# Performance work log

Hardware: AMD Instinct MI355X
Metric: run time of the kernel (lower is better)

Reference implementation:

```python
import jax, jax.numpy as jnp
import numpy as np

N_NODES = 50000
N_EDGES = 1600000
D_FEAT = 128
EPS = 1e-12  # matches F.normalize clamp_min eps


def setup_inputs() -> dict:
    key = jax.random.key(0)
    k1, k2 = jax.random.split(key)
    x = jax.random.normal(k1, (N_NODES, D_FEAT), dtype=jnp.float32)
    beta = jnp.ones((1,), dtype=jnp.float32)  # AGNNConv learnable scalar, init 1.0
    edge_index = jax.random.randint(k2, (2, N_EDGES), 0, N_NODES, dtype=jnp.int64)
    return {"x": x, "beta": beta, "edge_index": edge_index}


def reference(x, beta, edge_index):
    N = x.shape[0]
    # AGNNConv default add_self_loops=True
    loop = jnp.arange(N, dtype=edge_index.dtype)
    src = jnp.concatenate([edge_index[0], loop])  # j (source / message sender)
    dst = jnp.concatenate([edge_index[1], loop])  # i (target / aggregator)

    # cosine-similarity attention logits per edge, scaled by beta
    xn = x * jax.lax.rsqrt(jnp.maximum(jnp.sum(x * x, axis=-1, keepdims=True), EPS * EPS))
    logits = beta[0] * jnp.sum(xn[src] * xn[dst], axis=-1)  # [E+N]

    # segment softmax over incoming edges of each target node
    m = jax.ops.segment_max(logits, dst, num_segments=N)
    m = jax.lax.stop_gradient(m)
    e = jnp.exp(logits - m[dst])
    s = jax.ops.segment_sum(e, dst, num_segments=N)
    alpha = e / s[dst]  # self-loops guarantee s > 0

    # scatter-aggregate messages alpha_e * x_src
    out = jax.ops.segment_sum(alpha[:, None] * x[src], dst, num_segments=N)

    # wrapper: activation (relu); normalization=False; dropout p=0 -> identity
    return jax.nn.relu(out)
```

## Files before the change

### kernel.cpp

```cpp
#include <hip/hip_runtime.h>

#define NN 50000
#define NE 1600000
#define DF 128
#define NB 250
#define BSZ 200
#define NWG 256
#define CHK 6250
#define NBN 12500

static __device__ __forceinline__ float bflo(unsigned int u) {
    unsigned int v = u << 16; float f; __builtin_memcpy(&f, &v, 4); return f;
}
static __device__ __forceinline__ float bfhi(unsigned int u) {
    unsigned int v = u & 0xFFFF0000u; float f; __builtin_memcpy(&f, &v, 4); return f;
}
static __device__ __forceinline__ unsigned int f2bf(float f) {
    unsigned int u; __builtin_memcpy(&u, &f, 4);
    u += 0x7FFFu + ((u >> 16) & 1u);
    return u >> 16;
}

static __device__ __forceinline__ int block_excl_scan(int v, int t, int* wsum4) {
    int lane = t & 63, wv = t >> 6;
    int s = v;
    #pragma unroll
    for (int off = 1; off < 64; off <<= 1) {
        int u = __shfl_up(s, off);
        if (lane >= off) s += u;
    }
    if (lane == 63) wsum4[wv] = s;
    __syncthreads();
    int add = 0;
    #pragma unroll
    for (int w = 0; w < 4; ++w) add += (w < wv) ? wsum4[w] : 0;
    __syncthreads();
    return s + add - v;
}

__global__ void k_norm_count(const float* __restrict__ x,
                             const int* __restrict__ ei,
                             unsigned int* __restrict__ xn_bf,
                             float* __restrict__ norm,
                             int* __restrict__ whist) {
    if (blockIdx.x < NBN) {
        int wave = (blockIdx.x * 256 + threadIdx.x) >> 6;
        int lane = threadIdx.x & 63;
        float2 v = ((const float2*)(x + (size_t)wave * DF))[lane];
        float ss = v.x * v.x + v.y * v.y;
        #pragma unroll
        for (int m = 1; m < 64; m <<= 1) ss += __shfl_xor(ss, m);
        float rinv = rsqrtf(fmaxf(ss, 1e-24f));
        xn_bf[(size_t)wave * 64 + lane] = (f2bf(v.y * rinv) << 16) | f2bf(v.x * rinv);
        if (lane == 0) norm[wave] = ss * rinv;
    } else {
        __shared__ int h[NB];
        int wg = blockIdx.x - NBN, t = threadIdx.x;
        if (t < NB) h[t] = 0;
        __syncthreads();
        const int* dstp = ei + NE + wg * CHK;
        for (int i = t; i < CHK; i += 256) atomicAdd(&h[dstp[i] / BSZ], 1);
        __syncthreads();
        if (t < NB) whist[wg * NB + t] = h[t];
    }
}

__global__ void k_scan(int* __restrict__ whist, int* __restrict__ btotal) {
    __shared__ int wsum4[4];
    int b = blockIdx.x, t = threadIdx.x;
    int v = whist[t * NB + b];
    int excl = block_excl_scan(v, t, wsum4);
    whist[t * NB + b] = excl;
    if (t == NWG - 1) btotal[b] = excl + v;
}

__global__ void k_part(const int* __restrict__ ei, const int* __restrict__ whist,
                       const int* __restrict__ btotal, unsigned int* __restrict__ pairs) {
    __shared__ int wsum4[4];
    __shared__ int cur[NB];
    int wg = blockIdx.x, t = threadIdx.x;
    int v = (t < NB) ? btotal[t] : 0;
    int base = block_excl_scan(v, t, wsum4);
    if (t < NB) cur[t] = base + whist[wg * NB + t];
    __syncthreads();
    int c0 = wg * CHK;
    for (int i = t; i < CHK; i += 256) {
        int src = ei[c0 + i];
        int dst = ei[NE + c0 + i];
        int b = dst / BSZ;
        int pos = atomicAdd(&cur[b], 1);
        pairs[pos] = ((unsigned int)(dst - b * BSZ) << 16) | (unsigned int)src;
    }
}

__global__ void k_build(const unsigned int* __restrict__ pairs,
                        const int* __restrict__ btotal,
                        const float* __restrict__ norm,
                        int* __restrict__ row_ptr, unsigned int* __restrict__ col) {
    __shared__ int wsum4[4];
    __shared__ int h[BSZ];
    __shared__ int sbase, send;
    int b = blockIdx.x, t = threadIdx.x;
    int v = (t < NB) ? btotal[t] : 0;
    int base_t = block_excl_scan(v, t, wsum4);
    if (t == b) { sbase = base_t; send = base_t + v; }
    if (t < BSZ) h[t] = 0;
    __syncthreads();
    int base = sbase, end = send;
    for (int i = base + t; i < end; i += 256) atomicAdd(&h[pairs[i] >> 16], 1);
    __syncthreads();
    int own = (t < BSZ) ? h[t] : 0;
    __syncthreads();
    int excl = block_excl_scan(own, t, wsum4);
    if (t < BSZ) {
        row_ptr[b * BSZ + t] = base + excl;
        h[t] = base + excl;
    }
    if (b == 0 && t == 0) row_ptr[NN] = NE;
    __syncthreads();
    for (int i = base + t; i < end; i += 256) {
        unsigned int p = pairs[i];
        unsigned int src = p & 0xFFFFu;
        int pos = atomicAdd(&h[p >> 16], 1);
        col[pos] = (f2bf(norm[src]) << 16) | src;
    }
}

__global__ void k_gather(const unsigned int* __restrict__ xn_bf,
                         const float* __restrict__ norm,
                         const int* __restrict__ row_ptr,
                         const unsigned int* __restrict__ col,
                         const float* __restrict__ beta_p,
                         float* __restrict__ out) {
    int wave = (blockIdx.x * blockDim.x + threadIdx.x) >> 6;
    int lane = threadIdx.x & 63;
    if (wave >= NN) return;
    int j = lane & 15;
    int g = lane >> 4;
    float beta = beta_p[0];
    float c = -fabsf(beta);

    uint4 du = ((const uint4*)(xn_bf + (size_t)wave * 64))[j];
    float xd[8];
    #pragma unroll
    for (int q = 0; q < 4; ++q) {
        unsigned int u = (&du.x)[q];
        xd[2 * q]     = bflo(u);
        xd[2 * q + 1] = bfhi(u);
    }

    float acc[8] = {0.f, 0.f, 0.f, 0.f, 0.f, 0.f, 0.f, 0.f};
    float ssum = 0.f;
    int b0 = row_ptr[wave], b1 = row_ptr[wave + 1];

    int k = b0 + g;
    int kA = (k     < b1) ? k     : 0;
    int kB = (k + 4 < b1) ? k + 4 : 0;
    unsigned int pA = col[kA];
    unsigned int pB = col[kB];
    uint4 rA = ((const uint4*)(xn_bf + (size_t)(pA & 0xFFFFu) * 64))[j];
    uint4 rB = ((const uint4*)(xn_bf + (size_t)(pB & 0xFFFFu) * 64))[j];

    for (; k < b1; k += 8) {
        int kC = (k +  8 < b1) ? k +  8 : 0;
        int kD = (k + 12 < b1) ? k + 12 : 0;
        unsigned int pC = col[kC];
        unsigned int pD = col[kD];
        uint4 rC = ((const uint4*)(xn_bf + (size_t)(pC & 0xFFFFu) * 64))[j];
        uint4 rD = ((const uint4*)(xn_bf + (size_t)(pD & 0xFFFFu) * 64))[j];

        {
            float xs[8];
            #pragma unroll
            for (int q = 0; q < 4; ++q) {
                unsigned int u = (&rA.x)[q];
                xs[2 * q]     = bflo(u);
                xs[2 * q + 1] = bfhi(u);
            }
            float dot = 0.f;
            #pragma unroll
            for (int q = 0; q < 8; ++q) dot = fmaf(xd[q], xs[q], dot);
            dot += __shfl_xor(dot, 1);
            dot += __shfl_xor(dot, 2);
            dot += __shfl_xor(dot, 4);
            dot += __shfl_xor(dot, 8);
            float e = __expf(fmaf(beta, dot, c));
            ssum += e;
            float w = e * bfhi(pA);
            #pragma unroll
            for (int q = 0; q < 8; ++q) acc[q] = fmaf(w, xs[q], acc[q]);
        }
        {
            float xs[8];
            #pragma unroll
            for (int q = 0; q < 4; ++q) {
                unsigned int u = (&rB.x)[q];
                xs[2 * q]     = bflo(u);
                xs[2 * q + 1] = bfhi(u);
            }
            float dot = 0.f;
            #pragma unroll
            for (int q = 0; q < 8; ++q) dot = fmaf(xd[q], xs[q], dot);
            dot += __shfl_xor(dot, 1);
            dot += __shfl_xor(dot, 2);
            dot += __shfl_xor(dot, 4);
            dot += __shfl_xor(dot, 8);
            float e = __expf(fmaf(beta, dot, c));
            e = (k + 4 < b1) ? e : 0.f;
            ssum += e;
            float w = e * bfhi(pB);
            #pragma unroll
            for (int q = 0; q < 8; ++q) acc[q] = fmaf(w, xs[q], acc[q]);
        }
        pA = pC; pB = pD; rA = rC; rB = rD;
    }

    ssum += __shfl_xor(ssum, 16);
    ssum += __shfl_xor(ssum, 32);
    #pragma unroll
    for (int q = 0; q < 8; ++q) {
        acc[q] += __shfl_xor(acc[q], 16);
        acc[q] += __shfl_xor(acc[q], 32);
    }

    float e_self = __expf(beta + c);
    ssum += e_self;
    float wsl = e_self * norm[wave];
    #pragma unroll
    for (int q = 0; q < 8; ++q) acc[q] = fmaf(wsl, xd[q], acc[q]);

    if (g == 0) {
        float inv = 1.0f / ssum;
        float4 o0, o1;
        o0.x = fmaxf(0.f, acc[0] * inv); o0.y = fmaxf(0.f, acc[1] * inv);
        o0.z = fmaxf(0.f, acc[2] * inv); o0.w = fmaxf(0.f, acc[3] * inv);
        o1.x = fmaxf(0.f, acc[4] * inv); o1.y = fmaxf(0.f, acc[5] * inv);
        o1.z = fmaxf(0.f, acc[6] * inv); o1.w = fmaxf(0.f, acc[7] * inv);
        float4* op = (float4*)(out + (size_t)wave * DF + 8 * j);
        op[0] = o0;
        op[1] = o1;
    }
}

extern "C" void kernel_launch(void* const* d_in, const int* in_sizes, int n_in,
                              void* d_out, int out_size, void* d_ws, size_t ws_size,
                              hipStream_t stream) {
    const float* x    = (const float*)d_in[0];
    const float* beta = (const float*)d_in[1];
    const int*   ei   = (const int*)d_in[2];
    float*       out  = (float*)d_out;

    char* ws = (char*)d_ws;
    unsigned int* xn_bf = (unsigned int*)ws;
    float* norm    = (float*)(ws + 12800000);
    int*   whist   = (int*)  (ws + 13000000);
    int*   btotal  = (int*)  (ws + 13256000);
    int*   row_ptr = (int*)  (ws + 13257024);
    unsigned int* pairs = (unsigned int*)(ws + 13457040);
    unsigned int* col   = (unsigned int*)(ws + 19857040);

    k_norm_count<<<NBN + NWG, 256, 0, stream>>>(x, ei, xn_bf, norm, whist);
    k_scan      <<<NB,        NWG, 0, stream>>>(whist, btotal);
    k_part      <<<NWG,       256, 0, stream>>>(ei, whist, btotal, pairs);
    k_build     <<<NB,        256, 0, stream>>>(pairs, btotal, norm, row_ptr, col);
    k_gather    <<<(NN * 64 + 255) / 256, 256, 0, stream>>>(xn_bf, norm, row_ptr, col, beta, out);
}
```

Measured before the change: 177.5 us.

## Fuse all stages into one cooperative persistent kernel with grid syncs

After: 669.2 us. +276.9%, slower.

```diff
diff --git a/kernel.cpp b/kernel.cpp
--- a/kernel.cpp
+++ b/kernel.cpp
@@ -1,4 +1,7 @@
 #include <hip/hip_runtime.h>
+#include <hip/hip_cooperative_groups.h>
+
+namespace cg = cooperative_groups;
 
 #define NN 50000
 #define NE 1600000
@@ -7,7 +10,6 @@
 #define BSZ 200
 #define NWG 256
 #define CHK 6250
-#define NBN 12500
 
 static __device__ __forceinline__ float bflo(unsigned int u) {
     unsigned int v = u << 16; float f; __builtin_memcpy(&f, &v, 4); return f;
@@ -38,207 +40,210 @@
     return s + add - v;
 }
 
-__global__ void k_norm_count(const float* __restrict__ x,
-                             const int* __restrict__ ei,
-                             unsigned int* __restrict__ xn_bf,
-                             float* __restrict__ norm,
-                             int* __restrict__ whist) {
-    if (blockIdx.x < NBN) {
-        int wave = (blockIdx.x * 256 + threadIdx.x) >> 6;
-        int lane = threadIdx.x & 63;
-        float2 v = ((const float2*)(x + (size_t)wave * DF))[lane];
-        float ss = v.x * v.x + v.y * v.y;
-        #pragma unroll
-        for (int m = 1; m < 64; m <<= 1) ss += __shfl_xor(ss, m);
-        float rinv = rsqrtf(fmaxf(ss, 1e-24f));
-        xn_bf[(size_t)wave * 64 + lane] = (f2bf(v.y * rinv) << 16) | f2bf(v.x * rinv);
-        if (lane == 0) norm[wave] = ss * rinv;
-    } else {
-        __shared__ int h[NB];
-        int wg = blockIdx.x - NBN, t = threadIdx.x;
-        if (t < NB) h[t] = 0;
-        __syncthreads();
-        const int* dstp = ei + NE + wg * CHK;
-        for (int i = t; i < CHK; i += 256) atomicAdd(&h[dstp[i] / BSZ], 1);
-        __syncthreads();
-        if (t < NB) whist[wg * NB + t] = h[t];
-    }
-}
-
-__global__ void k_scan(int* __restrict__ whist, int* __restrict__ btotal) {
+__global__ __launch_bounds__(256, 8)
+void k_mega(const float* __restrict__ x, const float* __restrict__ beta_p,
+            const int* __restrict__ ei,
+            unsigned int* __restrict__ xn_bf, float* __restrict__ norm,
+            int* __restrict__ whist, int* __restrict__ btotal,
+            int* __restrict__ row_ptr, unsigned int* __restrict__ pairs,
+            unsigned int* __restrict__ col, float* __restrict__ out) {
+    cg::grid_group grid = cg::this_grid();
     __shared__ int wsum4[4];
-    int b = blockIdx.x, t = threadIdx.x;
-    int v = whist[t * NB + b];
-    int excl = block_excl_scan(v, t, wsum4);
-    whist[t * NB + b] = excl;
-    if (t == NWG - 1) btotal[b] = excl + v;
-}
-
-__global__ void k_part(const int* __restrict__ ei, const int* __restrict__ whist,
-                       const int* __restrict__ btotal, unsigned int* __restrict__ pairs) {
-    __shared__ int wsum4[4];
-    __shared__ int cur[NB];
-    int wg = blockIdx.x, t = threadIdx.x;
-    int v = (t < NB) ? btotal[t] : 0;
-    int base = block_excl_scan(v, t, wsum4);
-    if (t < NB) cur[t] = base + whist[wg * NB + t];
-    __syncthreads();
-    int c0 = wg * CHK;
-    for (int i = t; i < CHK; i += 256) {
-        int src = ei[c0 + i];
-        int dst = ei[NE + c0 + i];
-        int b = dst / BSZ;
-        int pos = atomicAdd(&cur[b], 1);
-        pairs[pos] = ((unsigned int)(dst - b * BSZ) << 16) | (unsigned int)src;
-    }
-}
-
-__global__ void k_build(const unsigned int* __restrict__ pairs,
-                        const int* __restrict__ btotal,
-                        const float* __restrict__ norm,
-                        int* __restrict__ row_ptr, unsigned int* __restrict__ col) {
-    __shared__ int wsum4[4];
-    __shared__ int h[BSZ];
+    __shared__ int smem[NB];
     __shared__ int sbase, send;
-    int b = blockIdx.x, t = threadIdx.x;
-    int v = (t < NB) ? btotal[t] : 0;
-    int base_t = block_excl_scan(v, t, wsum4);
-    if (t == b) { sbase = base_t; send = base_t + v; }
-    if (t < BSZ) h[t] = 0;
-    __syncthreads();
-    int base = sbase, end = send;
-    for (int i = base + t; i < end; i += 256) atomicAdd(&h[pairs[i] >> 16], 1);
-    __syncthreads();
-    int own = (t < BSZ) ? h[t] : 0;
-    __syncthreads();
-    int excl = block_excl_scan(own, t, wsum4);
-    if (t < BSZ) {
-        row_ptr[b * BSZ + t] = base + excl;
-        h[t] = base + excl;
-    }
-    if (b == 0 && t == 0) row_ptr[NN] = NE;
-    __syncthreads();
-    for (int i = base + t; i < end; i += 256) {
-        unsigned int p = pairs[i];
-        unsigned int src = p & 0xFFFFu;
-        int pos = atomicAdd(&h[p >> 16], 1);
-        col[pos] = (f2bf(norm[src]) << 16) | src;
-    }
-}
-
-__global__ void k_gather(const unsigned int* __restrict__ xn_bf,
-                         const float* __restrict__ norm,
-                         const int* __restrict__ row_ptr,
-                         const unsigned int* __restrict__ col,
-                         const float* __restrict__ beta_p,
-                         float* __restrict__ out) {
-    int wave = (blockIdx.x * blockDim.x + threadIdx.x) >> 6;
-    int lane = threadIdx.x & 63;
-    if (wave >= NN) return;
-    int j = lane & 15;
-    int g = lane >> 4;
-    float beta = beta_p[0];
-    float c = -fabsf(beta);
-
-    uint4 du = ((const uint4*)(xn_bf + (size_t)wave * 64))[j];
-    float xd[8];
-    #pragma unroll
-    for (int q = 0; q < 4; ++q) {
-        unsigned int u = (&du.x)[q];
-        xd[2 * q]     = bflo(u);
-        xd[2 * q + 1] = bfhi(u);
-    }
-
-    float acc[8] = {0.f, 0.f, 0.f, 0.f, 0.f, 0.f, 0.f, 0.f};
-    float ssum = 0.f;
-    int b0 = row_ptr[wave], b1 = row_ptr[wave + 1];
-
-    int k = b0 + g;
-    int kA = (k     < b1) ? k     : 0;
-    int kB = (k + 4 < b1) ? k + 4 : 0;
-    unsigned int pA = col[kA];
-    unsigned int pB = col[kB];
-    uint4 rA = ((const uint4*)(xn_bf + (size_t)(pA & 0xFFFFu) * 64))[j];
-    uint4 rB = ((const uint4*)(xn_bf + (size_t)(pB & 0xFFFFu) * 64))[j];
-
-    for (; k < b1; k += 8) {
-        int kC = (k +  8 < b1) ? k +  8 : 0;
-        int kD = (k + 12 < b1) ? k + 12 : 0;
-        unsigned int pC = col[kC];
-        unsigned int pD = col[kD];
-        uint4 rC = ((const uint4*)(xn_bf + (size_t)(pC & 0xFFFFu) * 64))[j];
-        uint4 rD = ((const uint4*)(xn_bf + (size_t)(pD & 0xFFFFu) * 64))[j];
-
-        {
-            float xs[8];
+    const int t = threadIdx.x;
+    const int bid = blockIdx.x;
+    const int nblk = gridDim.x;
+
+    {
+        bool split = (nblk >= NWG + 256);
+        bool do_count = (bid < NWG);
+        bool do_norm = split ? (bid >= NWG) : true;
+        if (do_norm) {
+            int nbid = split ? bid - NWG : bid;
+            int nnb  = split ? nblk - NWG : nblk;
+            int lane = t & 63;
+            int w0 = nbid * 4 + (t >> 6);
+            int wstep = nnb * 4;
+            for (int node = w0; node < NN; node += wstep) {
+                float2 v = ((const float2*)(x + (size_t)node * DF))[lane];
+                float ss = v.x * v.x + v.y * v.y;
+                #pragma unroll
+                for (int m = 1; m < 64; m <<= 1) ss += __shfl_xor(ss, m);
+                float rinv = rsqrtf(fmaxf(ss, 1e-24f));
+                xn_bf[(size_t)node * 64 + lane] = (f2bf(v.y * rinv) << 16) | f2bf(v.x * rinv);
+                if (lane == 0) norm[node] = ss * rinv;
+            }
+        }
+        if (do_count) {
+            if (t < NB) smem[t] = 0;
+            __syncthreads();
+            const int* dstp = ei + NE + bid * CHK;
+            for (int i = t; i < CHK; i += 256) atomicAdd(&smem[dstp[i] / BSZ], 1);
+            __syncthreads();
+            if (t < NB) whist[bid * NB + t] = smem[t];
+        }
+    }
+    grid.sync();
+
+    if (bid < NB) {
+        int v = whist[t * NB + bid];
+        int excl = block_excl_scan(v, t, wsum4);
+        whist[t * NB + bid] = excl;
+        if (t == NWG - 1) btotal[bid] = excl + v;
+    }
+    grid.sync();
+
+    if (bid < NWG) {
+        int v = (t < NB) ? btotal[t] : 0;
+        int base = block_excl_scan(v, t, wsum4);
+        if (t < NB) smem[t] = base + whist[bid * NB + t];
+        __syncthreads();
+        int c0 = bid * CHK;
+        for (int i = t; i < CHK; i += 256) {
+            int src = ei[c0 + i];
+            int dst = ei[NE + c0 + i];
+            int b = dst / BSZ;
+            int pos = atomicAdd(&smem[b], 1);
+            pairs[pos] = ((unsigned int)(dst - b * BSZ) << 16) | (unsigned int)src;
+        }
+    }
+    grid.sync();
+
+    if (bid < NB) {
+        int v = (t < NB) ? btotal[t] : 0;
+        int base_t = block_excl_scan(v, t, wsum4);
+        if (t == bid) { sbase = base_t; send = base_t + v; }
+        if (t < BSZ) smem[t] = 0;
+        __syncthreads();
+        int base = sbase, end = send;
+        for (int i = base + t; i < end; i += 256) atomicAdd(&smem[pairs[i] >> 16], 1);
+        __syncthreads();
+        int own = (t < BSZ) ? smem[t] : 0;
+        __syncthreads();
+        int excl = block_excl_scan(own, t, wsum4);
+        if (t < BSZ) {
+            row_ptr[bid * BSZ + t] = base + excl;
+            smem[t] = base + excl;
+        }
+        if (bid == 0 && t == 0) row_ptr[NN] = NE;
+        __syncthreads();
+        for (int i = base + t; i < end; i += 256) {
+            unsigned int p = pairs[i];
+            unsigned int src = p & 0xFFFFu;
+            int pos = atomicAdd(&smem[p >> 16], 1);
+            col[pos] = (f2bf(norm[src]) << 16) | src;
+        }
+    }
+    grid.sync();
+
+    {
+        int lane = t & 63;
+        int j = lane & 15;
+        int g = lane >> 4;
+        float beta = beta_p[0];
+        float c = -fabsf(beta);
+        int gw = bid * 4 + (t >> 6);
+        int gstep = nblk * 4;
+        for (int node = gw; node < NN; node += gstep) {
+            uint4 du = ((const uint4*)(xn_bf + (size_t)node * 64))[j];
+            float xd[8];
             #pragma unroll
             for (int q = 0; q < 4; ++q) {
-                unsigned int u = (&rA.x)[q];
-                xs[2 * q]     = bflo(u);
-                xs[2 * q + 1] = bfhi(u);
-            }
-            float dot = 0.f;
+                unsigned int u = (&du.x)[q];
+                xd[2 * q]     = bflo(u);
+                xd[2 * q + 1] = bfhi(u);
+            }
+            float acc[8] = {0.f, 0.f, 0.f, 0.f, 0.f, 0.f, 0.f, 0.f};
+            float ssum = 0.f;
+            int b0 = row_ptr[node], b1 = row_ptr[node + 1];
+
+            int k = b0 + g;
+            int kA = (k     < b1) ? k     : 0;
+            int kB = (k + 4 < b1) ? k + 4 : 0;
+            unsigned int pA = col[kA];
+            unsigned int pB = col[kB];
+            uint4 rA = ((const uint4*)(xn_bf + (size_t)(pA & 0xFFFFu) * 64))[j];
+            uint4 rB = ((const uint4*)(xn_bf + (size_t)(pB & 0xFFFFu) * 64))[j];
+
+            for (; k < b1; k += 8) {
+                int kC = (k +  8 < b1) ? k +  8 : 0;
+                int kD = (k + 12 < b1) ? k + 12 : 0;
+                unsigned int pC = col[kC];
+                unsigned int pD = col[kD];
+                uint4 rC = ((const uint4*)(xn_bf + (size_t)(pC & 0xFFFFu) * 64))[j];
+                uint4 rD = ((const uint4*)(xn_bf + (size_t)(pD & 0xFFFFu) * 64))[j];
+                {
+                    float xs[8];
+                    #pragma unroll
+                    for (int q = 0; q < 4; ++q) {
+                        unsigned int u = (&rA.x)[q];
+                        xs[2 * q]     = bflo(u);
+                        xs[2 * q + 1] = bfhi(u);
+                    }
+                    float dot = 0.f;
+                    #pragma unroll
+                    for (int q = 0; q < 8; ++q) dot = fmaf(xd[q], xs[q], dot);
+                    dot += __shfl_xor(dot, 1);
+                    dot += __shfl_xor(dot, 2);
+                    dot += __shfl_xor(dot, 4);
+                    dot += __shfl_xor(dot, 8);
+                    float e = __expf(fmaf(beta, dot, c));
+                    ssum += e;
+                    float w = e * bfhi(pA);
+                    #pragma unroll
+                    for (int q = 0; q < 8; ++q) acc[q] = fmaf(w, xs[q], acc[q]);
+                }
+                {
+                    float xs[8];
+                    #pragma unroll
+                    for (int q = 0; q < 4; ++q) {
+                        unsigned int u = (&rB.x)[q];
+                        xs[2 * q]     = bflo(u);
+                        xs[2 * q + 1] = bfhi(u);
+                    }
+                    float dot = 0.f;
+                    #pragma unroll
+                    for (int q = 0; q < 8; ++q) dot = fmaf(xd[q], xs[q], dot);
+                    dot += __shfl_xor(dot, 1);
+                    dot += __shfl_xor(dot, 2);
+                    dot += __shfl_xor(dot, 4);
+                    dot += __shfl_xor(dot, 8);
+                    float e = __expf(fmaf(beta, dot, c));
+                    e = (k + 4 < b1) ? e : 0.f;
+                    ssum += e;
+                    float w = e * bfhi(pB);
+                    #pragma unroll
+                    for (int q = 0; q < 8; ++q) acc[q] = fmaf(w, xs[q], acc[q]);
+                }
+                pA = pC; pB = pD; rA = rC; rB = rD;
+            }
+
+            ssum += __shfl_xor(ssum, 16);
+            ssum += __shfl_xor(ssum, 32);
             #pragma unroll
-            for (int q = 0; q < 8; ++q) dot = fmaf(xd[q], xs[q], dot);
-            dot += __shfl_xor(dot, 1);
-            dot += __shfl_xor(dot, 2);
-            dot += __shfl_xor(dot, 4);
-            dot += __shfl_xor(dot, 8);
-            float e = __expf(fmaf(beta, dot, c));
-            ssum += e;
-            float w = e * bfhi(pA);
+            for (int q = 0; q < 8; ++q) {
+                acc[q] += __shfl_xor(acc[q], 16);
+                acc[q] += __shfl_xor(acc[q], 32);
+            }
+            float e_self = __expf(beta + c);
+            ssum += e_self;
+            float wsl = e_self * norm[node];
             #pragma unroll
-            for (int q = 0; q < 8; ++q) acc[q] = fmaf(w, xs[q], acc[q]);
-        }
-        {
-            float xs[8];
-            #pragma unroll
-            for (int q = 0; q < 4; ++q) {
-                unsigned int u = (&rB.x)[q];
-                xs[2 * q]     = bflo(u);
-                xs[2 * q + 1] = bfhi(u);
-            }
-            float dot = 0.f;
-            #pragma unroll
-            for (int q = 0; q < 8; ++q) dot = fmaf(xd[q], xs[q], dot);
-            dot += __shfl_xor(dot, 1);
-            dot += __shfl_xor(dot, 2);
-            dot += __shfl_xor(dot, 4);
-            dot += __shfl_xor(dot, 8);
-            float e = __expf(fmaf(beta, dot, c));
-            e = (k + 4 < b1) ? e : 0.f;
-            ssum += e;
-            float w = e * bfhi(pB);
-            #pragma unroll
-            for (int q = 0; q < 8; ++q) acc[q] = fmaf(w, xs[q], acc[q]);
-        }
-        pA = pC; pB = pD; rA = rC; rB = rD;
-    }
-
-    ssum += __shfl_xor(ssum, 16);
-    ssum += __shfl_xor(ssum, 32);
-    #pragma unroll
-    for (int q = 0; q < 8; ++q) {
-        acc[q] += __shfl_xor(acc[q], 16);
-        acc[q] += __shfl_xor(acc[q], 32);
-    }
-
-    float e_self = __expf(beta + c);
-    ssum += e_self;
-    float wsl = e_self * norm[wave];
-    #pragma unroll
-    for (int q = 0; q < 8; ++q) acc[q] = fmaf(wsl, xd[q], acc[q]);
-
-    if (g == 0) {
-        float inv = 1.0f / ssum;
-        float4 o0, o1;
-        o0.x = fmaxf(0.f, acc[0] * inv); o0.y = fmaxf(0.f, acc[1] * inv);
-        o0.z = fmaxf(0.f, acc[2] * inv); o0.w = fmaxf(0.f, acc[3] * inv);
-        o1.x = fmaxf(0.f, acc[4] * inv); o1.y = fmaxf(0.f, acc[5] * inv);
-        o1.z = fmaxf(0.f, acc[6] * inv); o1.w = fmaxf(0.f, acc[7] * inv);
-        float4* op = (float4*)(out + (size_t)wave * DF + 8 * j);
-        op[0] = o0;
-        op[1] = o1;
+            for (int q = 0; q < 8; ++q) acc[q] = fmaf(wsl, xd[q], acc[q]);
+
+            if (g == 0) {
+                float inv = 1.0f / ssum;
+                float4 o0, o1;
+                o0.x = fmaxf(0.f, acc[0] * inv); o0.y = fmaxf(0.f, acc[1] * inv);
+                o0.z = fmaxf(0.f, acc[2] * inv); o0.w = fmaxf(0.f, acc[3] * inv);
+                o1.x = fmaxf(0.f, acc[4] * inv); o1.y = fmaxf(0.f, acc[5] * inv);
+                o1.z = fmaxf(0.f, acc[6] * inv); o1.w = fmaxf(0.f, acc[7] * inv);
+                float4* op = (float4*)(out + (size_t)node * DF + 8 * j);
+                op[0] = o0;
+                op[1] = o1;
+            }
+        }
     }
 }
 
@@ -259,9 +264,21 @@
     unsigned int* pairs = (unsigned int*)(ws + 13457040);
     unsigned int* col   = (unsigned int*)(ws + 19857040);
 
-    k_norm_count<<<NBN + NWG, 256, 0, stream>>>(x, ei, xn_bf, norm, whist);
-    k_scan      <<<NB,        NWG, 0, stream>>>(whist, btotal);
-    k_part      <<<NWG,       256, 0, stream>>>(ei, whist, btotal, pairs);
-    k_build     <<<NB,        256, 0, stream>>>(pairs, btotal, norm, row_ptr, col);
-    k_gather    <<<(NN * 64 + 255) / 256, 256, 0, stream>>>(xn_bf, norm, row_ptr, col, beta, out);
-}
+    int dev = 0;
+    hipGetDevice(&dev);
+    int nb = 0;
+    hipOccupancyMaxActiveBlocksPerMultiprocessor(&nb, (const void*)k_mega, 256, 0);
+    if (nb < 1) nb = 1;
+    int ncu = 0;
+    hipDeviceGetAttribute(&ncu, hipDeviceAttributeMultiprocessorCount, dev);
+    if (ncu < 1) ncu = 256;
+    long grid = (long)nb * ncu;
+    if (grid > 2048) grid = 2048;
+    if (grid < NWG) grid = NWG;
+
+    void* args[] = { (void*)&x, (void*)&beta, (void*)&ei,
+                     (void*)&xn_bf, (void*)&norm, (void*)&whist, (void*)&btotal,
+                     (void*)&row_ptr, (void*)&pairs, (void*)&col, (void*)&out };
+    hipLaunchCooperativeKernel((const void*)k_mega, dim3((unsigned)grid), dim3(256),
+                               args, 0, stream);
+}
```

## Fuse CSR build into gather using fixed-capacity buckets and global atomics

Applied to the files above, without the earlier changes.

Result: slower. 193.2 us (+8.8%).

```diff
diff --git a/kernel.cpp b/kernel.cpp
--- a/kernel.cpp
+++ b/kernel.cpp
@@ -3,10 +3,11 @@
 #define NN 50000
 #define NE 1600000
 #define DF 128
-#define NB 250
-#define BSZ 200
-#define NWG 256
-#define CHK 6250
+#define NB 1250
+#define BSZ 40
+#define CAP 1664
+#define NWGP 512
+#define CHKP 3125
 #define NBN 12500
 
 static __device__ __forceinline__ float bflo(unsigned int u) {
@@ -21,224 +22,192 @@
     return u >> 16;
 }
 
-static __device__ __forceinline__ int block_excl_scan(int v, int t, int* wsum4) {
-    int lane = t & 63, wv = t >> 6;
-    int s = v;
-    #pragma unroll
-    for (int off = 1; off < 64; off <<= 1) {
-        int u = __shfl_up(s, off);
-        if (lane >= off) s += u;
-    }
-    if (lane == 63) wsum4[wv] = s;
-    __syncthreads();
-    int add = 0;
-    #pragma unroll
-    for (int w = 0; w < 4; ++w) add += (w < wv) ? wsum4[w] : 0;
-    __syncthreads();
-    return s + add - v;
-}
-
-__global__ void k_norm_count(const float* __restrict__ x,
-                             const int* __restrict__ ei,
-                             unsigned int* __restrict__ xn_bf,
-                             float* __restrict__ norm,
-                             int* __restrict__ whist) {
+__global__ void k_norm_part(const float* __restrict__ x,
+                            const int* __restrict__ ei,
+                            unsigned int* __restrict__ xn_bf,
+                            float* __restrict__ norm,
+                            int* __restrict__ gcnt,
+                            unsigned int* __restrict__ pairs) {
     if (blockIdx.x < NBN) {
-        int wave = (blockIdx.x * 256 + threadIdx.x) >> 6;
+        int node = (blockIdx.x * 256 + threadIdx.x) >> 6;
         int lane = threadIdx.x & 63;
-        float2 v = ((const float2*)(x + (size_t)wave * DF))[lane];
+        float2 v = ((const float2*)(x + (size_t)node * DF))[lane];
         float ss = v.x * v.x + v.y * v.y;
         #pragma unroll
         for (int m = 1; m < 64; m <<= 1) ss += __shfl_xor(ss, m);
         float rinv = rsqrtf(fmaxf(ss, 1e-24f));
-        xn_bf[(size_t)wave * 64 + lane] = (f2bf(v.y * rinv) << 16) | f2bf(v.x * rinv);
-        if (lane == 0) norm[wave] = ss * rinv;
+        xn_bf[(size_t)node * 64 + lane] = (f2bf(v.y * rinv) << 16) | f2bf(v.x * rinv);
+        if (lane == 0) norm[node] = ss * rinv;
     } else {
         __shared__ int h[NB];
         int wg = blockIdx.x - NBN, t = threadIdx.x;
-        if (t < NB) h[t] = 0;
+        for (int i = t; i < NB; i += 256) h[i] = 0;
         __syncthreads();
-        const int* dstp = ei + NE + wg * CHK;
-        for (int i = t; i < CHK; i += 256) atomicAdd(&h[dstp[i] / BSZ], 1);
+        const int* dstp = ei + NE + wg * CHKP;
+        const int* srcp = ei + wg * CHKP;
+        for (int i = t; i < CHKP; i += 256) atomicAdd(&h[dstp[i] / BSZ], 1);
         __syncthreads();
-        if (t < NB) whist[wg * NB + t] = h[t];
-    }
-}
-
-__global__ void k_scan(int* __restrict__ whist, int* __restrict__ btotal) {
-    __shared__ int wsum4[4];
+        for (int i = t; i < NB; i += 256) {
+            int c = h[i];
+            int base = (c > 0) ? atomicAdd(&gcnt[i], c) : 0;
+            h[i] = i * CAP + base;
+        }
+        __syncthreads();
+        for (int i = t; i < CHKP; i += 256) {
+            int src = srcp[i];
+            int dst = dstp[i];
+            int b = dst / BSZ;
+            int pos = atomicAdd(&h[b], 1);
+            if (pos < (b + 1) * CAP)
+                pairs[pos] = ((unsigned int)(dst - b * BSZ) << 16) | (unsigned int)src;
+        }
+    }
+}
+
+__global__ __launch_bounds__(256)
+void k_build_gather(const unsigned int* __restrict__ xn_bf,
+                    const float* __restrict__ norm,
+                    const int* __restrict__ gcnt,
+                    const unsigned int* __restrict__ pairs,
+                    const float* __restrict__ beta_p,
+                    float* __restrict__ out) {
+    __shared__ unsigned int colL[CAP];
+    __shared__ int hist[BSZ];
+    __shared__ int rp[BSZ + 1];
     int b = blockIdx.x, t = threadIdx.x;
-    int v = whist[t * NB + b];
-    int excl = block_excl_scan(v, t, wsum4);
-    whist[t * NB + b] = excl;
-    if (t == NWG - 1) btotal[b] = excl + v;
-}
-
-__global__ void k_part(const int* __restrict__ ei, const int* __restrict__ whist,
-                       const int* __restrict__ btotal, unsigned int* __restrict__ pairs) {
-    __shared__ int wsum4[4];
-    __shared__ int cur[NB];
-    int wg = blockIdx.x, t = threadIdx.x;
-    int v = (t < NB) ? btotal[t] : 0;
-    int base = block_excl_scan(v, t, wsum4);
-    if (t < NB) cur[t] = base + whist[wg * NB + t];
-    __syncthreads();
-    int c0 = wg * CHK;
-    for (int i = t; i < CHK; i += 256) {
-        int src = ei[c0 + i];
-        int dst = ei[NE + c0 + i];
-        int b = dst / BSZ;
-        int pos = atomicAdd(&cur[b], 1);
-        pairs[pos] = ((unsigned int)(dst - b * BSZ) << 16) | (unsigned int)src;
-    }
-}
-
-__global__ void k_build(const unsigned int* __restrict__ pairs,
-                        const int* __restrict__ btotal,
-                        const float* __restrict__ norm,
-                        int* __restrict__ row_ptr, unsigned int* __restrict__ col) {
-    __shared__ int wsum4[4];
-    __shared__ int h[BSZ];
-    __shared__ int sbase, send;
-    int b = blockIdx.x, t = threadIdx.x;
-    int v = (t < NB) ? btotal[t] : 0;
-    int base_t = block_excl_scan(v, t, wsum4);
-    if (t == b) { sbase = base_t; send = base_t + v; }
-    if (t < BSZ) h[t] = 0;
-    __syncthreads();
-    int base = sbase, end = send;
-    for (int i = base + t; i < end; i += 256) atomicAdd(&h[pairs[i] >> 16], 1);
-    __syncthreads();
-    int own = (t < BSZ) ? h[t] : 0;
-    __syncthreads();
-    int excl = block_excl_scan(own, t, wsum4);
-    if (t < BSZ) {
-        row_ptr[b * BSZ + t] = base + excl;
-        h[t] = base + excl;
-    }
-    if (b == 0 && t == 0) row_ptr[NN] = NE;
-    __syncthreads();
-    for (int i = base + t; i < end; i += 256) {
-        unsigned int p = pairs[i];
+    int cnt = gcnt[b];
+    if (cnt > CAP) cnt = CAP;
+    int base = b * CAP;
+
+    if (t < BSZ) hist[t] = 0;
+    __syncthreads();
+    for (int i = t; i < cnt; i += 256) atomicAdd(&hist[pairs[base + i] >> 16], 1);
+    __syncthreads();
+    if (t < 64) {
+        int v = (t < BSZ) ? hist[t] : 0;
+        int s = v;
+        #pragma unroll
+        for (int off = 1; off < 64; off <<= 1) {
+            int u = __shfl_up(s, off);
+            if (t >= off) s += u;
+        }
+        if (t < BSZ) { rp[t + 1] = s; hist[t] = s - v; }
+        if (t == 0) rp[0] = 0;
+    }
+    __syncthreads();
+    for (int i = t; i < cnt; i += 256) {
+        unsigned int p = pairs[base + i];
         unsigned int src = p & 0xFFFFu;
-        int pos = atomicAdd(&h[p >> 16], 1);
-        col[pos] = (f2bf(norm[src]) << 16) | src;
-    }
-}
-
-__global__ void k_gather(const unsigned int* __restrict__ xn_bf,
-                         const float* __restrict__ norm,
-                         const int* __restrict__ row_ptr,
-                         const unsigned int* __restrict__ col,
-                         const float* __restrict__ beta_p,
-                         float* __restrict__ out) {
-    int wave = (blockIdx.x * blockDim.x + threadIdx.x) >> 6;
-    int lane = threadIdx.x & 63;
-    if (wave >= NN) return;
+        int pos = atomicAdd(&hist[p >> 16], 1);
+        colL[pos] = (f2bf(norm[src]) << 16) | src;
+    }
+    __syncthreads();
+
+    int lane = t & 63;
+    int w = t >> 6;
     int j = lane & 15;
     int g = lane >> 4;
     float beta = beta_p[0];
     float c = -fabsf(beta);
-
-    uint4 du = ((const uint4*)(xn_bf + (size_t)wave * 64))[j];
-    float xd[8];
-    #pragma unroll
-    for (int q = 0; q < 4; ++q) {
-        unsigned int u = (&du.x)[q];
-        xd[2 * q]     = bflo(u);
-        xd[2 * q + 1] = bfhi(u);
-    }
-
-    float acc[8] = {0.f, 0.f, 0.f, 0.f, 0.f, 0.f, 0.f, 0.f};
-    float ssum = 0.f;
-    int b0 = row_ptr[wave], b1 = row_ptr[wave + 1];
-
-    int k = b0 + g;
-    int kA = (k     < b1) ? k     : 0;
-    int kB = (k + 4 < b1) ? k + 4 : 0;
-    unsigned int pA = col[kA];
-    unsigned int pB = col[kB];
-    uint4 rA = ((const uint4*)(xn_bf + (size_t)(pA & 0xFFFFu) * 64))[j];
-    uint4 rB = ((const uint4*)(xn_bf + (size_t)(pB & 0xFFFFu) * 64))[j];
-
-    for (; k < b1; k += 8) {
-        int kC = (k +  8 < b1) ? k +  8 : 0;
-        int kD = (k + 12 < b1) ? k + 12 : 0;
-        unsigned int pC = col[kC];
-        unsigned int pD = col[kD];
-        uint4 rC = ((const uint4*)(xn_bf + (size_t)(pC & 0xFFFFu) * 64))[j];
-        uint4 rD = ((const uint4*)(xn_bf + (size_t)(pD & 0xFFFFu) * 64))[j];
-
-        {
-            float xs[8];
-            #pragma unroll
-            for (int q = 0; q < 4; ++q) {
-                unsigned int u = (&rA.x)[q];
-                xs[2 * q]     = bflo(u);
-                xs[2 * q + 1] = bfhi(u);
+    for (int ln = w; ln < BSZ; ln += 4) {
+        int node = b * BSZ + ln;
+        uint4 du = ((const uint4*)(xn_bf + (size_t)node * 64))[j];
+        float xd[8];
+        #pragma unroll
+        for (int q = 0; q < 4; ++q) {
+            unsigned int u = (&du.x)[q];
+            xd[2 * q]     = bflo(u);
+            xd[2 * q + 1] = bfhi(u);
+        }
+        float acc[8] = {0.f, 0.f, 0.f, 0.f, 0.f, 0.f, 0.f, 0.f};
+        float ssum = 0.f;
+        int b0 = rp[ln], b1 = rp[ln + 1];
+
+        int k = b0 + g;
+        int kA = (k     < b1) ? k     : 0;
+        int kB = (k + 4 < b1) ? k + 4 : 0;
+        unsigned int pA = colL[kA];
+        unsigned int pB = colL[kB];
+        uint4 rA = ((const uint4*)(xn_bf + (size_t)(pA & 0xFFFFu) * 64))[j];
+        uint4 rB = ((const uint4*)(xn_bf + (size_t)(pB & 0xFFFFu) * 64))[j];
+
+        for (; k < b1; k += 8) {
+            int kC = (k +  8 < b1) ? k +  8 : 0;
+            int kD = (k + 12 < b1) ? k + 12 : 0;
+            unsigned int pC = colL[kC];
+            unsigned int pD = colL[kD];
+            uint4 rC = ((const uint4*)(xn_bf + (size_t)(pC & 0xFFFFu) * 64))[j];
+            uint4 rD = ((const uint4*)(xn_bf + (size_t)(pD & 0xFFFFu) * 64))[j];
+            {
+                float xs[8];
+                #pragma unroll
+                for (int q = 0; q < 4; ++q) {
+                    unsigned int u = (&rA.x)[q];
+                    xs[2 * q]     = bflo(u);
+                    xs[2 * q + 1] = bfhi(u);
+                }
+                float dot = 0.f;
+                #pragma unroll
+                for (int q = 0; q < 8; ++q) dot = fmaf(xd[q], xs[q], dot);
+                dot += __shfl_xor(dot, 1);
+                dot += __shfl_xor(dot, 2);
+                dot += __shfl_xor(dot, 4);
+                dot += __shfl_xor(dot, 8);
+                float e = __expf(fmaf(beta, dot, c));
+                ssum += e;
+                float wgt = e * bfhi(pA);
+                #pragma unroll
+                for (int q = 0; q < 8; ++q) acc[q] = fmaf(wgt, xs[q], acc[q]);
             }
-            float dot = 0.f;
-            #pragma unroll
-            for (int q = 0; q < 8; ++q) dot = fmaf(xd[q], xs[q], dot);
-            dot += __shfl_xor(dot, 1);
-            dot += __shfl_xor(dot, 2);
-            dot += __shfl_xor(dot, 4);
-            dot += __shfl_xor(dot, 8);
-            float e = __expf(fmaf(beta, dot, c));
-            ssum += e;
-            float w = e * bfhi(pA);
-            #pragma unroll
-            for (int q = 0; q < 8; ++q) acc[q] = fmaf(w, xs[q], acc[q]);
-        }
-        {
-            float xs[8];
-            #pragma unroll
-            for (int q = 0; q < 4; ++q) {
-                unsigned int u = (&rB.x)[q];
-                xs[2 * q]     = bflo(u);
-                xs[2 * q + 1] = bfhi(u);
+            {
+                float xs[8];
+                #pragma unroll
+                for (int q = 0; q < 4; ++q) {
+                    unsigned int u = (&rB.x)[q];
+                    xs[2 * q]     = bflo(u);
+                    xs[2 * q + 1] = bfhi(u);
+                }
+                float dot = 0.f;
+                #pragma unroll
+                for (int q = 0; q < 8; ++q) dot = fmaf(xd[q], xs[q], dot);
+                dot += __shfl_xor(dot, 1);
+                dot += __shfl_xor(dot, 2);
+                dot += __shfl_xor(dot, 4);
+                dot += __shfl_xor(dot, 8);
+                float e = __expf(fmaf(beta, dot, c));
+                e = (k + 4 < b1) ? e : 0.f;
+                ssum += e;
+                float wgt = e * bfhi(pB);
+                #pragma unroll
+                for (int q = 0; q < 8; ++q) acc[q] = fmaf(wgt, xs[q], acc[q]);
             }
-            float dot = 0.f;
-            #pragma unroll
-            for (int q = 0; q < 8; ++q) dot = fmaf(xd[q], xs[q], dot);
-            dot += __shfl_xor(dot, 1);
-            dot += __shfl_xor(dot, 2);
-            dot += __shfl_xor(dot, 4);
-            dot += __shfl_xor(dot, 8);
-            float e = __expf(fmaf(beta, dot, c));
-            e = (k + 4 < b1) ? e : 0.f;
-            ssum += e;
-            float w = e * bfhi(pB);
-            #pragma unroll
-            for (int q = 0; q < 8; ++q) acc[q] = fmaf(w, xs[q], acc[q]);
-        }
-        pA = pC; pB = pD; rA = rC; rB = rD;
-    }
-
-    ssum += __shfl_xor(ssum, 16);
-    ssum += __shfl_xor(ssum, 32);
-    #pragma unroll
-    for (int q = 0; q < 8; ++q) {
-        acc[q] += __shfl_xor(acc[q], 16);
-        acc[q] += __shfl_xor(acc[q], 32);
-    }
-
-    float e_self = __expf(beta + c);
-    ssum += e_self;
-    float wsl = e_self * norm[wave];
-    #pragma unroll
-    for (int q = 0; q < 8; ++q) acc[q] = fmaf(wsl, xd[q], acc[q]);
-
-    if (g == 0) {
-        float inv = 1.0f / ssum;
-        float4 o0, o1;
-        o0.x = fmaxf(0.f, acc[0] * inv); o0.y = fmaxf(0.f, acc[1] * inv);
-        o0.z = fmaxf(0.f, acc[2] * inv); o0.w = fmaxf(0.f, acc[3] * inv);
-        o1.x = fmaxf(0.f, acc[4] * inv); o1.y = fmaxf(0.f, acc[5] * inv);
-        o1.z = fmaxf(0.f, acc[6] * inv); o1.w = fmaxf(0.f, acc[7] * inv);
-        float4* op = (float4*)(out + (size_t)wave * DF + 8 * j);
-        op[0] = o0;
-        op[1] = o1;
+            pA = pC; pB = pD; rA = rC; rB = rD;
+        }
+
+        ssum += __shfl_xor(ssum, 16);
+        ssum += __shfl_xor(ssum, 32);
+        #pragma unroll
+        for (int q = 0; q < 8; ++q) {
+            acc[q] += __shfl_xor(acc[q], 16);
+            acc[q] += __shfl_xor(acc[q], 32);
+        }
+        float e_self = __expf(beta + c);
+        ssum += e_self;
+        float wsl = e_self * norm[node];
+        #pragma unroll
+        for (int q = 0; q < 8; ++q) acc[q] = fmaf(wsl, xd[q], acc[q]);
+
+        if (g == 0) {
+            float inv = 1.0f / ssum;
+            float4 o0, o1;
+            o0.x = fmaxf(0.f, acc[0] * inv); o0.y = fmaxf(0.f, acc[1] * inv);
+            o0.z = fmaxf(0.f, acc[2] * inv); o0.w = fmaxf(0.f, acc[3] * inv);
+            o1.x = fmaxf(0.f, acc[4] * inv); o1.y = fmaxf(0.f, acc[5] * inv);
+            o1.z = fmaxf(0.f, acc[6] * inv); o1.w = fmaxf(0.f, acc[7] * inv);
+            float4* op = (float4*)(out + (size_t)node * DF + 8 * j);
+            op[0] = o0;
+            op[1] = o1;
+        }
     }
 }
 
@@ -252,16 +221,11 @@
 
     char* ws = (char*)d_ws;
     unsigned int* xn_bf = (unsigned int*)ws;
-    float* norm    = (float*)(ws + 12800000);
-    int*   whist   = (int*)  (ws + 13000000);
-    int*   btotal  = (int*)  (ws + 13256000);
-    int*   row_ptr = (int*)  (ws + 13257024);
-    unsigned int* pairs = (unsigned int*)(ws + 13457040);
-    unsigned int* col   = (unsigned int*)(ws + 19857040);
-
-    k_norm_count<<<NBN + NWG, 256, 0, stream>>>(x, ei, xn_bf, norm, whist);
-    k_scan      <<<NB,        NWG, 0, stream>>>(whist, btotal);
-    k_part      <<<NWG,       256, 0, stream>>>(ei, whist, btotal, pairs);
-    k_build     <<<NB,        256, 0, stream>>>(pairs, btotal, norm, row_ptr, col);
-    k_gather    <<<(NN * 64 + 255) / 256, 256, 0, stream>>>(xn_bf, norm, row_ptr, col, beta, out);
-}
+    float* norm = (float*)(ws + 12800000);
+    int*   gcnt = (int*)  (ws + 13000000);
+    unsigned int* pairs = (unsigned int*)(ws + 13005056);
+
+    hipMemsetAsync(gcnt, 0, NB * sizeof(int), stream);
+    k_norm_part  <<<NBN + NWGP, 256, 0, stream>>>(x, ei, xn_bf, norm, gcnt, pairs);
+    k_build_gather<<<NB,        256, 0, stream>>>(xn_bf, norm, gcnt, pairs, beta, out);
+}
```
